# Optimization experiments

Measured on AMD Instinct MI355X. Metric: run time of the kernel, lower is better.

The kernel has to match this reference:

```python
import jax, jax.numpy as jnp
import numpy as np

VJ = 80      # vjointnum (groups)
FS = 480     # feature_size = 2*k of RFF
HD = 256     # hidden_dim
K = 240      # RFF k
BATCH = 2048
TWO_PI = 2.0 * np.pi
SLOPE = 0.01  # LeakyReLU default negative_slope


def _wn(v, g):
    # weight_norm (dim=0): w[o,:] = g[o] * v[o,:] / ||v[o,:]||
    return v * (g[:, None] / jnp.linalg.norm(v, axis=1, keepdims=True))


def _grouped(x, v, g, b):
    # x: [B, G, in_g]; v: [G*out_g, in_g]; equivalent to groups=G Conv1d with kernel 1
    w = _wn(v, g)
    out_g = w.shape[0] // VJ
    y = jnp.einsum('bgi,goi->bgo', x, w.reshape(VJ, out_g, -1))
    return y + b.reshape(VJ, out_g)


def _lrelu(t):
    return jnp.where(t >= 0, t, SLOPE * t)


def setup_inputs() -> dict:
    key = jax.random.key(0)
    ks = jax.random.split(key, 12)
    d = {
        'querypoint': jax.random.normal(ks[0], (BATCH, VJ, 3), jnp.float32),
        'point_features': jax.random.normal(ks[1], (BATCH, VJ, FS), jnp.float32),
        'B_rff': jax.random.normal(ks[2], (3, K), jnp.float32),  # std=1
    }
    # per-group layer sizes: 480->512, 512->512, 512->256, 256->6
    dims = [(FS, 2 * HD), (2 * HD, 2 * HD), (2 * HD, HD), (HD, 6)]
    for i, (din, dout) in enumerate(dims):
        d[f'v{i}'] = jax.random.normal(ks[3 + 2 * i], (VJ * dout, din), jnp.float32) * 0.02
        d[f'g{i}'] = jnp.ones((VJ * dout,), jnp.float32)
        d[f'b{i}'] = jnp.zeros((VJ * dout,), jnp.float32)
    return d


def reference(querypoint, point_features, B_rff,
              v0, g0, b0, v1, g1, b1, v2, g2, b2, v3, g3, b3):
    # RFF encode: [B, N, 480]
    emb = TWO_PI * jnp.einsum('bnd,dk->bnk', querypoint, B_rff)
    feat = jnp.concatenate([jnp.cos(emb), jnp.sin(emb)], axis=-1)
    x = point_features + feat                       # [B, 80, 480]
    Bsz = x.shape[0]
    # transpose(-2,-1) then reshape(B, C*N, 1) with groups=80 ==> [B, 80, 480]
    x = jnp.transpose(x, (0, 2, 1)).reshape(Bsz, VJ, FS)
    x = _lrelu(_grouped(x, v0, g0, b0))             # [B, 80, 512]
    x = _lrelu(_grouped(x, v1, g1, b1))             # [B, 80, 512]
    x = _lrelu(_grouped(x, v2, g2, b2))             # [B, 80, 256]
    y = _grouped(x, v3, g3, b3)                     # [B, 80, 6]
    return y.reshape(Bsz, VJ, 6)
```

## Files before the change

kernel.cpp:

```cpp
#include <hip/hip_runtime.h>


typedef __attribute__((ext_vector_type(8)))  short short8;
typedef __attribute__((ext_vector_type(4)))  float f32x4;
typedef __attribute__((ext_vector_type(16))) float f32x16;
typedef __attribute__((ext_vector_type(2)))  unsigned int uint2v;

#define VJ    80
#define FS    480
#define HD2   512
#define HD    256
#define BATCH 2048
#define SMLP  520

static __device__ __forceinline__ unsigned short f2bf(float f) {
  unsigned int u = __builtin_bit_cast(unsigned int, f);
  u += 0x7FFFu + ((u >> 16) & 1u);
  return (unsigned short)(u >> 16);
}

template<int K, int RPG>
static __device__ __forceinline__ void wfrag32_body(
    int blk, const float* __restrict__ v, const float* __restrict__ gain,
    unsigned short* __restrict__ dst, float* sV, float* sScale) {
  constexpr int KS = K / 16;
  constexpr int KP = K + 4;
  const int t  = threadIdx.x;
  const int n0 = blk * 32;
  const int g  = n0 / RPG;
  const int nt = (n0 % RPG) >> 5;

  const f32x4* v4 = (const f32x4*)(v + (size_t)n0 * K);
  for (int idx = t; idx < 32 * K / 4; idx += 1024) {
    int row = idx / (K / 4), rem = idx - row * (K / 4);
    *(f32x4*)&sV[row * KP + rem * 4] = v4[idx];
  }
  __syncthreads();

  const int wave = t >> 6, lane = t & 63;
  for (int r = wave; r < 32; r += 16) {
    float s = 0.f;
    for (int k = lane; k < K; k += 64) { float x = sV[r * KP + k]; s += x * x; }
    #pragma unroll
    for (int off = 32; off > 0; off >>= 1) s += __shfl_down(s, off);
    if (lane == 0) sScale[r] = gain[n0 + r] / sqrtf(s);
  }
  __syncthreads();

  unsigned short* db = dst + (size_t)g * RPG * K + (size_t)nt * KS * 512;
  for (int o = t; o < KS * 64; o += 1024) {
    int ks = o >> 6, l = o & 63;
    int nl = l & 31, k0 = ks * 16 + ((l >> 5) << 3);
    float sc = sScale[nl];
    short8 pk;
    #pragma unroll
    for (int j = 0; j < 8; ++j) pk[j] = (short)f2bf(sV[nl * KP + k0 + j] * sc);
    *(short8*)&db[(size_t)ks * 512 + l * 8] = pk;
  }
}

static __device__ __forceinline__ void w3frag_body(
    int gidx, const float* __restrict__ v3, const float* __restrict__ g3,
    unsigned short* __restrict__ W3f, float* sV, float* sScale) {
  const int t = threadIdx.x;
  const f32x4* v4 = (const f32x4*)(v3 + (size_t)gidx * 6 * 256);
  if (t < 384) {
    int row = t >> 6, rem = t & 63;
    *(f32x4*)&sV[row * 260 + rem * 4] = v4[t];
  }
  __syncthreads();
  const int wave = t >> 6, lane = t & 63;
  if (wave < 6) {
    float s = 0.f;
    #pragma unroll
    for (int k = 0; k < 4; ++k) { float x = sV[wave * 260 + lane + k * 64]; s += x * x; }
    #pragma unroll
    for (int off = 32; off > 0; off >>= 1) s += __shfl_down(s, off);
    if (lane == 0) sScale[wave] = g3[gidx * 6 + wave] / sqrtf(s);
  }
  __syncthreads();
  if (t < 512) {
    int ks = t >> 6, l = t & 63;
    int c = l & 15, k0 = ks * 32 + ((l >> 4) << 3);
    short8 pk;
    #pragma unroll
    for (int j = 0; j < 8; ++j)
      pk[j] = (c < 6) ? (short)f2bf(sV[c * 260 + k0 + j] * sScale[c]) : (short)0;
    *(short8*)&W3f[(size_t)gidx * 4096 + (size_t)ks * 512 + l * 8] = pk;
  }
}

static __device__ __forceinline__ void prep_x_body(
    int b, const float* __restrict__ qp, const float* __restrict__ pf,
    const float* __restrict__ Brff, unsigned short* __restrict__ Xg,
    float* sB, float* sQ, unsigned short* sX) {
  const int t = threadIdx.x;
  if (t < 720) sB[t] = Brff[t];
  if (t < 240) sQ[t] = qp[(size_t)b * 240 + t];
  __syncthreads();
  const float* pfb = pf + (size_t)b * 38400;
  #pragma unroll 2
  for (int idx = t; idx < 9600; idx += 1024) {
    int n2 = idx / 240;
    int c2 = idx - n2 * 240;
    int n  = n2 * 2, c = c2 * 2;
    int k  = (c < 240) ? c : c - 240;
    float bx0 = sB[k],       bx1 = sB[k + 1];
    float by0 = sB[240 + k], by1 = sB[241 + k];
    float bz0 = sB[480 + k], bz1 = sB[481 + k];
    float qx0 = sQ[n*3],   qy0 = sQ[n*3+1], qz0 = sQ[n*3+2];
    float qx1 = sQ[n*3+3], qy1 = sQ[n*3+4], qz1 = sQ[n*3+5];
    float d00 = qx0 * bx0 + qy0 * by0 + qz0 * bz0;
    float d01 = qx0 * bx1 + qy0 * by1 + qz0 * bz1;
    float d10 = qx1 * bx0 + qy1 * by0 + qz1 * bz0;
    float d11 = qx1 * bx1 + qy1 * by1 + qz1 * bz1;
    bool ucos = (c < 240);
    float f00 = ucos ? __builtin_amdgcn_cosf(d00) : __builtin_amdgcn_sinf(d00);
    float f01 = ucos ? __builtin_amdgcn_cosf(d01) : __builtin_amdgcn_sinf(d01);
    float f10 = ucos ? __builtin_amdgcn_cosf(d10) : __builtin_amdgcn_sinf(d10);
    float f11 = ucos ? __builtin_amdgcn_cosf(d11) : __builtin_amdgcn_sinf(d11);
    float2 p0 = *(const float2*)&pfb[n * 480 + c];
    float2 p1 = *(const float2*)&pfb[(n + 1) * 480 + c];
    unsigned int w0 = (unsigned int)f2bf(p0.x + f00)
                    | ((unsigned int)f2bf(p1.x + f10) << 16);
    unsigned int w1 = (unsigned int)f2bf(p0.y + f01)
                    | ((unsigned int)f2bf(p1.y + f11) << 16);
    *(unsigned int*)&sX[c * 82 + n]       = w0;
    *(unsigned int*)&sX[(c + 1) * 82 + n] = w1;
  }
  __syncthreads();
  for (int idx4 = t; idx4 < 9600; idx4 += 1024) {
    int g  = idx4 / 120;
    int i4 = idx4 - g * 120;
    int i  = i4 * 4;
    int cl = i / 80;
    int n  = i - cl * 80;
    const unsigned int* p = (const unsigned int*)&sX[(g * 6 + cl) * 82 + n];
    uint2v val = { p[0], p[1] };
    *(uint2v*)(Xg + ((size_t)g * BATCH + b) * 480 + i) = val;
  }
}

__global__ void __launch_bounds__(1024)
prep_all(const float* __restrict__ qp, const float* __restrict__ pf,
         const float* __restrict__ Brff,
         const float* __restrict__ v0, const float* __restrict__ g0,
         const float* __restrict__ v1, const float* __restrict__ g1,
         const float* __restrict__ v2, const float* __restrict__ g2,
         const float* __restrict__ v3, const float* __restrict__ g3,
         unsigned short* __restrict__ W0, unsigned short* __restrict__ W1,
         unsigned short* __restrict__ W2, unsigned short* __restrict__ W3f,
         unsigned short* __restrict__ Xg) {
  __shared__ float sMem[960];
  __shared__ unsigned short sBig[480 * 82];
  const int bid = blockIdx.x;
  const int q = bid / 13, r = bid - q * 13;
  if (r < 8) {
    const int wb = q * 8 + r;
    float* sV = (float*)sBig;
    float* sScale = sMem;
    if      (wb < 1280) wfrag32_body<480, 512>(wb,        v0, g0, W0, sV, sScale);
    else if (wb < 2560) wfrag32_body<512, 512>(wb - 1280, v1, g1, W1, sV, sScale);
    else if (wb < 3200) wfrag32_body<512, 256>(wb - 2560, v2, g2, W2, sV, sScale);
    else if (wb < 3280) w3frag_body(wb - 3200, v3, g3, W3f, sV, sScale);
  } else {
    const int pb = q * 5 + (r - 8);
    if (pb < BATCH)
      prep_x_body(pb, qp, pf, Brff, Xg, sMem, sMem + 720, sBig);
  }
}

#define MLP_STEP32(ksv, BB)                                                   \
  {                                                                           \
    const int ksc = (ksv);                                                    \
    short8 a0 = *(const short8*)(aB + ksc * 16);                              \
    short8 a1 = *(const short8*)(aB + 32 * SMLP + ksc * 16);                  \
    short8 p0, p1;                                                            \
    const bool pf_ok = (ksc + 3 < KS);                                        \
    if (pf_ok) {                                                              \
      p0 = *(const short8*)(wB + ((size_t)0 * KS + ksc + 3) * 512);           \
      if (NT > 1) p1 = *(const short8*)(wB + ((size_t)1 * KS + ksc + 3) * 512); \
    }                                                                         \
    __builtin_amdgcn_s_setprio(1);                                            \
    _Pragma("unroll")                                                         \
    for (int nt = 0; nt < NT; ++nt)                                           \
      acc[0][nt] = __builtin_amdgcn_mfma_f32_32x32x16_bf16(a0, BB[nt], acc[0][nt], 0, 0, 0); \
    _Pragma("unroll")                                                         \
    for (int nt = 0; nt < NT; ++nt)                                           \
      acc[1][nt] = __builtin_amdgcn_mfma_f32_32x32x16_bf16(a1, BB[nt], acc[1][nt], 0, 0, 0); \
    __builtin_amdgcn_s_setprio(0);                                            \
    if (pf_ok) {                                                              \
      BB[0] = p0;                                                             \
      if (NT > 1) BB[1] = p1;                                                 \
    }                                                                         \
  }

template<int K, int N, bool ACT>
static __device__ __forceinline__ void run_layer32(
    unsigned short* __restrict__ s,
    const unsigned short* __restrict__ Wf, const float* __restrict__ bias,
    int wn, int lane) {
  constexpr int NT = N / 256;
  constexpr int KS = K / 16;
  const int nbase = wn * (N / 8);
  const int lr = lane & 31, lh = lane >> 5;

  f32x16 acc[2][NT];
  #pragma unroll
  for (int mt = 0; mt < 2; ++mt)
    #pragma unroll
    for (int nt = 0; nt < NT; ++nt)
      #pragma unroll
      for (int r = 0; r < 16; ++r) acc[mt][nt][r] = 0.f;

  const unsigned short* aB = s + lr * SMLP + lh * 8;
  const unsigned short* wB = Wf + (size_t)(wn * NT) * KS * 512 + lane * 8;

  short8 bb0[NT], bb1[NT], bb2[NT];
  #pragma unroll
  for (int nt = 0; nt < NT; ++nt) bb0[nt] = *(const short8*)(wB + ((size_t)nt * KS    ) * 512);
  #pragma unroll
  for (int nt = 0; nt < NT; ++nt) bb1[nt] = *(const short8*)(wB + ((size_t)nt * KS + 1) * 512);
  #pragma unroll
  for (int nt = 0; nt < NT; ++nt) bb2[nt] = *(const short8*)(wB + ((size_t)nt * KS + 2) * 512);

  #pragma unroll
  for (int ks3 = 0; ks3 < KS / 3; ++ks3) {
    MLP_STEP32(3 * ks3,     bb0);
    MLP_STEP32(3 * ks3 + 1, bb1);
    MLP_STEP32(3 * ks3 + 2, bb2);
  }
  if (KS % 3 == 2) {
    MLP_STEP32(KS - 2, bb0);
    MLP_STEP32(KS - 1, bb1);
  }

  float bv[NT];
  #pragma unroll
  for (int nt = 0; nt < NT; ++nt) bv[nt] = bias[nbase + nt * 32 + lr];

  __syncthreads();
  #pragma unroll
  for (int mt = 0; mt < 2; ++mt)
    #pragma unroll
    for (int nt = 0; nt < NT; ++nt)
      #pragma unroll
      for (int r = 0; r < 16; ++r) {
        float val = acc[mt][nt][r] + bv[nt];
        if (ACT) val = (val >= 0.f) ? val : 0.01f * val;
        const int row = mt * 32 + (r & 3) + 8 * (r >> 2) + 4 * lh;
        s[row * SMLP + (nbase + nt * 32 + lr)] = f2bf(val);
      }
  __syncthreads();
}

__global__ void __launch_bounds__(512, 4)
mlp_kernel(const unsigned short* __restrict__ Xg,
           const unsigned short* __restrict__ W0, const unsigned short* __restrict__ W1,
           const unsigned short* __restrict__ W2, const unsigned short* __restrict__ W3f,
           const float* __restrict__ b0, const float* __restrict__ b1,
           const float* __restrict__ b2, const float* __restrict__ b3,
           float* __restrict__ out) {
  __shared__ unsigned short s[64 * SMLP];

  const int bid   = blockIdx.x;
  const int xcd   = bid & 7;
  const int local = bid >> 3;
  const int g     = xcd * 10 + (local >> 5);
  const int tile  = local & 31;
  const int m0    = tile * 64;

  const int tid  = threadIdx.x, lane = tid & 63;
  const int wn   = tid >> 6;

  const unsigned short* Xs = Xg + ((size_t)g * BATCH + m0) * 480;
  for (int idx = tid; idx < 64 * 60; idx += 512) {
    int row = idx / 60, c = idx - row * 60;
    *(short8*)&s[row * SMLP + c * 8] = *(const short8*)(Xs + (size_t)row * 480 + c * 8);
  }
  __syncthreads();

  run_layer32<480, 512, true>(s, W0 + (size_t)g * 512 * 480, b0 + g * 512, wn, lane);
  run_layer32<512, 512, true>(s, W1 + (size_t)g * 512 * 512, b1 + g * 512, wn, lane);
  run_layer32<512, 256, true>(s, W2 + (size_t)g * 256 * 512, b2 + g * 256, wn, lane);

  if (wn < 4) {
    const int lr = lane & 15, lh = lane >> 4;
    const unsigned short* aB4 = s + (wn * 16 + lr) * SMLP + lh * 8;
    const unsigned short* w3  = W3f + (size_t)g * 4096 + lane * 8;
    f32x4 a4 = (f32x4){0.f, 0.f, 0.f, 0.f};
    #pragma unroll
    for (int kk = 0; kk < 8; ++kk) {
      short8 av  = *(const short8*)(aB4 + kk * 32);
      short8 wv8 = *(const short8*)(w3 + (size_t)kk * 512);
      a4 = __builtin_amdgcn_mfma_f32_16x16x32_bf16(av, wv8, a4, 0, 0, 0);
    }
    const int col = lane & 15;
    if (col < 6) {
      const float bias3 = b3[g * 6 + col];
      #pragma unroll
      for (int r = 0; r < 4; ++r)
        out[((size_t)(m0 + wn * 16 + lh * 4 + r) * VJ + g) * 6 + col] = a4[r] + bias3;
    }
  }
}

extern "C" void kernel_launch(void* const* d_in, const int* in_sizes, int n_in,
                              void* d_out, int out_size, void* d_ws, size_t ws_size,
                              hipStream_t stream) {
  const float* qp   = (const float*)d_in[0];
  const float* pf   = (const float*)d_in[1];
  const float* Brff = (const float*)d_in[2];
  const float* v0 = (const float*)d_in[3];  const float* g0 = (const float*)d_in[4];  const float* b0 = (const float*)d_in[5];
  const float* v1 = (const float*)d_in[6];  const float* g1 = (const float*)d_in[7];  const float* b1 = (const float*)d_in[8];
  const float* v2 = (const float*)d_in[9];  const float* g2 = (const float*)d_in[10]; const float* b2 = (const float*)d_in[11];
  const float* v3 = (const float*)d_in[12]; const float* g3 = (const float*)d_in[13]; const float* b3 = (const float*)d_in[14];

  unsigned short* W0  = (unsigned short*)d_ws;
  unsigned short* W1  = W0 + (size_t)VJ * HD2 * FS;
  unsigned short* W2  = W1 + (size_t)VJ * HD2 * HD2;
  unsigned short* W3f = W2 + (size_t)VJ * HD  * HD2;
  unsigned short* Xg  = W3f + (size_t)VJ * 4096;

  prep_all<<<dim3(5330), dim3(1024), 0, stream>>>(qp, pf, Brff,
                                                  v0, g0, v1, g1, v2, g2, v3, g3,
                                                  W0, W1, W2, W3f, Xg);
  mlp_kernel<<<dim3(VJ * 32), dim3(512), 0, stream>>>(Xg, W0, W1, W2, W3f,
                                                      b0, b1, b2, b3, (float*)d_out);
}
```

Before: 380.0 us.

## Double MLP row tile to 128 with 16 waves, one N-tile per wave

The MLP kernel now processes 128 batch rows per block with 1024 threads instead of 64 rows with 512 threads. Each wave owns a single 32-column N tile and iterates over several 32-row M tiles, so each weight fragment loaded from global memory is reused across more rows and total weight traffic is halved. In exchange the block uses twice the LDS (about 133KB), which limits occupancy to roughly one block per CU. Larger blocks also mean fewer blocks to spread across the GPU.

```diff
diff --git a/kernel.cpp b/kernel.cpp
--- a/kernel.cpp
+++ b/kernel.cpp
@@ -170,123 +170,110 @@
   }
 }
 
-#define MLP_STEP32(ksv, BB)                                                   \
+#define MLP_STEP16W(ksv, BB)                                                  \
   {                                                                           \
     const int ksc = (ksv);                                                    \
-    short8 a0 = *(const short8*)(aB + ksc * 16);                              \
-    short8 a1 = *(const short8*)(aB + 32 * SMLP + ksc * 16);                  \
-    short8 p0, p1;                                                            \
+    short8 a[MT];                                                             \
+    _Pragma("unroll")                                                         \
+    for (int mt = 0; mt < MT; ++mt)                                           \
+      a[mt] = *(const short8*)(aB + mt * 32 * SMLP + ksc * 16);               \
+    short8 p0;                                                                \
     const bool pf_ok = (ksc + 3 < KS);                                        \
-    if (pf_ok) {                                                              \
-      p0 = *(const short8*)(wB + ((size_t)0 * KS + ksc + 3) * 512);           \
-      if (NT > 1) p1 = *(const short8*)(wB + ((size_t)1 * KS + ksc + 3) * 512); \
-    }                                                                         \
+    if (pf_ok) p0 = *(const short8*)(wB + (size_t)(ksc + 3) * 512);           \
     __builtin_amdgcn_s_setprio(1);                                            \
     _Pragma("unroll")                                                         \
-    for (int nt = 0; nt < NT; ++nt)                                           \
-      acc[0][nt] = __builtin_amdgcn_mfma_f32_32x32x16_bf16(a0, BB[nt], acc[0][nt], 0, 0, 0); \
-    _Pragma("unroll")                                                         \
-    for (int nt = 0; nt < NT; ++nt)                                           \
-      acc[1][nt] = __builtin_amdgcn_mfma_f32_32x32x16_bf16(a1, BB[nt], acc[1][nt], 0, 0, 0); \
+    for (int mt = 0; mt < MT; ++mt)                                           \
+      acc[mt] = __builtin_amdgcn_mfma_f32_32x32x16_bf16(a[mt], BB, acc[mt], 0, 0, 0); \
     __builtin_amdgcn_s_setprio(0);                                            \
-    if (pf_ok) {                                                              \
-      BB[0] = p0;                                                             \
-      if (NT > 1) BB[1] = p1;                                                 \
-    }                                                                         \
+    if (pf_ok) BB = p0;                                                       \
   }
 
 template<int K, int N, bool ACT>
-static __device__ __forceinline__ void run_layer32(
+static __device__ __forceinline__ void run_layer16w(
     unsigned short* __restrict__ s,
     const unsigned short* __restrict__ Wf, const float* __restrict__ bias,
-    int wn, int lane) {
-  constexpr int NT = N / 256;
+    int wave, int lane) {
+  constexpr int WN = N / 32;
+  constexpr int MT = WN / 4;
   constexpr int KS = K / 16;
-  const int nbase = wn * (N / 8);
+  constexpr int KB3 = (KS / 3) * 3;
+  const int wn = wave & (WN - 1);
+  const int wm = wave / WN;
+  const int nbase = wn * 32;
   const int lr = lane & 31, lh = lane >> 5;
 
-  f32x16 acc[2][NT];
+  f32x16 acc[MT];
   #pragma unroll
-  for (int mt = 0; mt < 2; ++mt)
-    #pragma unroll
-    for (int nt = 0; nt < NT; ++nt)
-      #pragma unroll
-      for (int r = 0; r < 16; ++r) acc[mt][nt][r] = 0.f;
-
-  const unsigned short* aB = s + lr * SMLP + lh * 8;
-  const unsigned short* wB = Wf + (size_t)(wn * NT) * KS * 512 + lane * 8;
-
-  short8 bb0[NT], bb1[NT], bb2[NT];
+  for (int mt = 0; mt < MT; ++mt)
+    #pragma unroll
+    for (int r = 0; r < 16; ++r) acc[mt][r] = 0.f;
+
+  const unsigned short* aB = s + (wm * MT * 32 + lr) * SMLP + lh * 8;
+  const unsigned short* wB = Wf + (size_t)wn * KS * 512 + lane * 8;
+
+  short8 bb0 = *(const short8*)(wB);
+  short8 bb1 = *(const short8*)(wB + 512);
+  short8 bb2 = *(const short8*)(wB + 1024);
+
   #pragma unroll
-  for (int nt = 0; nt < NT; ++nt) bb0[nt] = *(const short8*)(wB + ((size_t)nt * KS    ) * 512);
+  for (int k3 = 0; k3 < KS / 3; ++k3) {
+    MLP_STEP16W(3 * k3,     bb0);
+    MLP_STEP16W(3 * k3 + 1, bb1);
+    MLP_STEP16W(3 * k3 + 2, bb2);
+  }
+  if (KS % 3 == 2) {
+    MLP_STEP16W(KB3,     bb0);
+    MLP_STEP16W(KB3 + 1, bb1);
+  }
+
+  const float bv = bias[nbase + lr];
+
+  __syncthreads();
   #pragma unroll
-  for (int nt = 0; nt < NT; ++nt) bb1[nt] = *(const short8*)(wB + ((size_t)nt * KS + 1) * 512);
-  #pragma unroll
-  for (int nt = 0; nt < NT; ++nt) bb2[nt] = *(const short8*)(wB + ((size_t)nt * KS + 2) * 512);
-
-  #pragma unroll
-  for (int ks3 = 0; ks3 < KS / 3; ++ks3) {
-    MLP_STEP32(3 * ks3,     bb0);
-    MLP_STEP32(3 * ks3 + 1, bb1);
-    MLP_STEP32(3 * ks3 + 2, bb2);
-  }
-  if (KS % 3 == 2) {
-    MLP_STEP32(KS - 2, bb0);
-    MLP_STEP32(KS - 1, bb1);
-  }
-
-  float bv[NT];
-  #pragma unroll
-  for (int nt = 0; nt < NT; ++nt) bv[nt] = bias[nbase + nt * 32 + lr];
-
-  __syncthreads();
-  #pragma unroll
-  for (int mt = 0; mt < 2; ++mt)
-    #pragma unroll
-    for (int nt = 0; nt < NT; ++nt)
-      #pragma unroll
-      for (int r = 0; r < 16; ++r) {
-        float val = acc[mt][nt][r] + bv[nt];
-        if (ACT) val = (val >= 0.f) ? val : 0.01f * val;
-        const int row = mt * 32 + (r & 3) + 8 * (r >> 2) + 4 * lh;
-        s[row * SMLP + (nbase + nt * 32 + lr)] = f2bf(val);
-      }
-  __syncthreads();
-}
-
-__global__ void __launch_bounds__(512, 4)
+  for (int mt = 0; mt < MT; ++mt)
+    #pragma unroll
+    for (int r = 0; r < 16; ++r) {
+      float val = acc[mt][r] + bv;
+      if (ACT) val = (val >= 0.f) ? val : 0.01f * val;
+      const int row = (wm * MT + mt) * 32 + (r & 3) + 8 * (r >> 2) + 4 * lh;
+      s[row * SMLP + nbase + lr] = f2bf(val);
+    }
+  __syncthreads();
+}
+
+__global__ void __launch_bounds__(1024, 4)
 mlp_kernel(const unsigned short* __restrict__ Xg,
            const unsigned short* __restrict__ W0, const unsigned short* __restrict__ W1,
            const unsigned short* __restrict__ W2, const unsigned short* __restrict__ W3f,
            const float* __restrict__ b0, const float* __restrict__ b1,
            const float* __restrict__ b2, const float* __restrict__ b3,
            float* __restrict__ out) {
-  __shared__ unsigned short s[64 * SMLP];
+  __shared__ unsigned short s[128 * SMLP];
 
   const int bid   = blockIdx.x;
   const int xcd   = bid & 7;
   const int local = bid >> 3;
-  const int g     = xcd * 10 + (local >> 5);
-  const int tile  = local & 31;
-  const int m0    = tile * 64;
+  const int g     = xcd * 10 + (local >> 4);
+  const int tile  = local & 15;
+  const int m0    = tile * 128;
 
   const int tid  = threadIdx.x, lane = tid & 63;
-  const int wn   = tid >> 6;
+  const int wave = tid >> 6;
 
   const unsigned short* Xs = Xg + ((size_t)g * BATCH + m0) * 480;
-  for (int idx = tid; idx < 64 * 60; idx += 512) {
+  for (int idx = tid; idx < 128 * 60; idx += 1024) {
     int row = idx / 60, c = idx - row * 60;
     *(short8*)&s[row * SMLP + c * 8] = *(const short8*)(Xs + (size_t)row * 480 + c * 8);
   }
   __syncthreads();
 
-  run_layer32<480, 512, true>(s, W0 + (size_t)g * 512 * 480, b0 + g * 512, wn, lane);
-  run_layer32<512, 512, true>(s, W1 + (size_t)g * 512 * 512, b1 + g * 512, wn, lane);
-  run_layer32<512, 256, true>(s, W2 + (size_t)g * 256 * 512, b2 + g * 256, wn, lane);
-
-  if (wn < 4) {
+  run_layer16w<480, 512, true>(s, W0 + (size_t)g * 512 * 480, b0 + g * 512, wave, lane);
+  run_layer16w<512, 512, true>(s, W1 + (size_t)g * 512 * 512, b1 + g * 512, wave, lane);
+  run_layer16w<512, 256, true>(s, W2 + (size_t)g * 256 * 512, b2 + g * 256, wave, lane);
+
+  if (wave < 8) {
     const int lr = lane & 15, lh = lane >> 4;
-    const unsigned short* aB4 = s + (wn * 16 + lr) * SMLP + lh * 8;
+    const unsigned short* aB4 = s + (wave * 16 + lr) * SMLP + lh * 8;
     const unsigned short* w3  = W3f + (size_t)g * 4096 + lane * 8;
     f32x4 a4 = (f32x4){0.f, 0.f, 0.f, 0.f};
     #pragma unroll
@@ -300,7 +287,7 @@
       const float bias3 = b3[g * 6 + col];
       #pragma unroll
       for (int r = 0; r < 4; ++r)
-        out[((size_t)(m0 + wn * 16 + lh * 4 + r) * VJ + g) * 6 + col] = a4[r] + bias3;
+        out[((size_t)(m0 + wave * 16 + lh * 4 + r) * VJ + g) * 6 + col] = a4[r] + bias3;
     }
   }
 }
@@ -325,6 +312,6 @@
   prep_all<<<dim3(5330), dim3(1024), 0, stream>>>(qp, pf, Brff,
                                                   v0, g0, v1, g1, v2, g2, v3, g3,
                                                   W0, W1, W2, W3f, Xg);
-  mlp_kernel<<<dim3(VJ * 32), dim3(512), 0, stream>>>(Xg, W0, W1, W2, W3f,
-                                                      b0, b1, b2, b3, (float*)d_out);
-}
+  mlp_kernel<<<dim3(VJ * 16), dim3(1024), 0, stream>>>(Xg, W0, W1, W2, W3f,
+                                                       b0, b1, b2, b3, (float*)d_out);
+}
```

Result: slower. 410.1 us (+7.9%).
